# Kernel optimization log

Hardware: AMD Instinct MI355X
Metric: run time of the kernel (lower is better)

The kernel has to match this reference:

```python
import jax, jax.numpy as jnp
import numpy as np

B, S, D, H = 2, 2048, 1024, 16
HD = D // H


def setup_inputs() -> dict:
    key = jax.random.key(0)
    ks = jax.random.split(key, 7)
    scale = 1.0 / np.sqrt(D)
    x = jax.random.normal(ks[0], (B, S, D), dtype=jnp.float32)
    att_mask = jax.random.randint(ks[1], (B, S, S), 0, 2, dtype=jnp.int32)
    Wq = jax.random.normal(ks[2], (D, D), dtype=jnp.float32) * scale
    Wk = jax.random.normal(ks[3], (D, D), dtype=jnp.float32) * scale
    Wv = jax.random.normal(ks[4], (D, D), dtype=jnp.float32) * scale
    Wo = jax.random.normal(ks[5], (D, D), dtype=jnp.float32) * scale
    bo = jnp.zeros((D,), dtype=jnp.float32)
    return {"x": x, "att_mask": att_mask, "Wq": Wq, "Wk": Wk, "Wv": Wv, "Wo": Wo, "bo": bo}


def reference(x, att_mask, Wq, Wk, Wv, Wo, bo):
    # Self-attention: kv_source = x, kv_len = q_len = S
    b, s, d = x.shape
    # projections; weights stored as (d_in, d_out)
    q = (x @ Wq).reshape(b, s, H, HD).transpose(0, 2, 1, 3)  # (B,H,S,HD)
    k = (x @ Wk).reshape(b, s, H, HD).transpose(0, 2, 1, 3)
    v = (x @ Wv).reshape(b, s, H, HD).transpose(0, 2, 1, 3)

    scores = jnp.einsum("bhqd,bhkd->bhqk", q, k) / jnp.sqrt(jnp.float32(HD))
    mask = att_mask.astype(bool)[:, None, :, :]  # (B,1,S,S)
    scores = jnp.where(mask, scores, -jnp.inf)

    # Recover fully-masked rows: set their first column score to 0.0
    all_masked = jnp.all(jnp.isneginf(scores), axis=-1, keepdims=True)  # (B,H,S,1)
    first_col = jnp.arange(s) == 0  # (S,)
    scores = jnp.where(all_masked & first_col, 0.0, scores)

    weights = jax.nn.softmax(scores, axis=-1)  # dropout is identity in eval mode
    ctx = jnp.einsum("bhqk,bhkd->bhqd", weights, v)  # (B,H,S,HD)
    ctx = ctx.transpose(0, 2, 1, 3).reshape(b, s, d)
    return ctx @ Wo + bo
```

## Files before the change

kernel.cpp:

```cpp
#include <hip/hip_runtime.h>
#include <stdint.h>

typedef unsigned short u16;
typedef unsigned int u32;
typedef __attribute__((ext_vector_type(8))) short bf16x8;
typedef __attribute__((ext_vector_type(4))) float f32x4;
typedef __attribute__((ext_vector_type(4))) u32 u32x4;

#define MFMA16(a, b, c) __builtin_amdgcn_mfma_f32_16x16x32_bf16((a), (b), (c), 0, 0, 0)

#define QSCALE 0.18033688011112042f

__device__ __forceinline__ u16 f2bf(float f) {
  u32 u = __float_as_uint(f);
  u += 0x7fffu + ((u >> 16) & 1u);
  return (u16)(u >> 16);
}

__device__ __forceinline__ u32 cvt_pk_bf16(float a, float b) {
  u32 r;
  asm("v_cvt_pk_bf16_f32 %0, %1, %2" : "=v"(r) : "v"(a), "v"(b));
  return r;
}

__device__ __forceinline__ void load_lds16(const void* g, void* l) {
  __builtin_amdgcn_global_load_lds((const __attribute__((address_space(1))) void*)g,
                                   (__attribute__((address_space(3))) void*)l, 16, 0, 0);
}

__device__ __forceinline__ int swz8(int row, int cb) {
  return row * 128 + ((cb ^ (row & 7)) << 4);
}

__global__ __launch_bounds__(256) void prep_kernel(const float4* __restrict__ x,
                                                   const int* __restrict__ mask,
                                                   const float* __restrict__ W0,
                                                   const float* __restrict__ W1,
                                                   const float* __restrict__ W2,
                                                   const float* __restrict__ W3,
                                                   ushort4* __restrict__ xbf,
                                                   u16* __restrict__ wt,
                                                   u32* __restrict__ MB) {
  const int bid = blockIdx.x, tid = threadIdx.x;
  __shared__ float t[32][33];
  __shared__ u32 nib[4][64];
  if (bid < 1024) {
    for (int i = bid * 256 + tid; i < 1048576; i += 262144) {
      float4 v = x[i];
      ushort4 o;
      o.x = f2bf(v.x); o.y = f2bf(v.y); o.z = f2bf(v.z); o.w = f2bf(v.w);
      xbf[i] = o;
    }
  } else if (bid < 5120) {
    int r = bid - 1024;
    const int z = r >> 10; r &= 1023;
    const int by = (r >> 5) << 5, bx = (r & 31) << 5;
    const float* W = (z == 0) ? W0 : (z == 1) ? W1 : (z == 2) ? W2 : W3;
    u16* o = wt + (size_t)z * 1048576;
    const int tx = tid & 31, ty = tid >> 5;
#pragma unroll
    for (int j = 0; j < 32; j += 8) t[ty + j][tx] = W[(size_t)(by + ty + j) * 1024 + bx + tx];
    __syncthreads();
#pragma unroll
    for (int j = 0; j < 32; j += 8) o[(size_t)(bx + ty + j) * 1024 + by + tx] = f2bf(t[tx][ty + j]);
  } else {
    const int wave = tid >> 6, lane = tid & 63;
    const int gw = (bid - 5120) * 4 + wave;
    for (int r = gw; r < 32768; r += 4096) {
      const int row = r >> 3, kb = (r & 7) << 8;
      int4 v = *(const int4*)(mask + (size_t)row * 2048 + kb + lane * 4);
      nib[wave][lane] = (v.x ? 1u : 0u) | (v.y ? 2u : 0u) | (v.z ? 4u : 0u) | (v.w ? 8u : 0u);
      if (lane < 8) {
        const u32* p = &nib[wave][lane << 3];
        u32 a = p[0] | (p[1] << 4) | (p[2] << 8) | (p[3] << 12) |
                (p[4] << 16) | (p[5] << 20) | (p[6] << 24) | (p[7] << 28);
        MB[(size_t)row * 64 + (kb >> 5) + lane] = a;
      }
    }
  }
}

template <int MODE>
__global__ __launch_bounds__(256) void gemm_kernel(const u16* __restrict__ A,
                                                   const u16* __restrict__ Bt,
                                                   u16* __restrict__ Qo, u16* __restrict__ Ko,
                                                   u16* __restrict__ Vo, float* __restrict__ Fo,
                                                   const float* __restrict__ bias) {
  __shared__ u16 As[128 * 64];
  __shared__ u16 Bs[128 * 64];
  const int tid = threadIdx.x, lane = tid & 63;
  const int l15 = lane & 15, g = lane >> 4;
  const int wave = tid >> 6, wr = wave >> 1, wc = wave & 1;
  const int L = blockIdx.x;
  const int xcd = L & 7, bi = L >> 3;
  int m0, n0;
  if (MODE == 0) {
    m0 = (((xcd & 3) << 3) + (bi & 7)) * 128;
    n0 = ((xcd >> 2) * 12 + (bi >> 3)) * 128;
  } else {
    m0 = ((xcd << 2) + (bi & 3)) * 128;
    n0 = (bi >> 2) * 128;
  }
  const int xo = (((tid & 7) ^ ((tid >> 3) & 7)) << 4);
  const char* Ag = (const char*)A + (size_t)(m0 + (tid >> 3)) * 2048 + xo;
  const char* Bg = (const char*)Bt + (size_t)(n0 + (tid >> 3)) * 2048 + xo;
  char* Asc = (char*)As;
  char* Bsc = (char*)Bs;
  char* ldA = Asc + wave * 1024;
  char* ldB = Bsc + wave * 1024;

  f32x4 acc[4][4] = {};

  for (int kt = 0; kt < 16; ++kt) {
    const int kbyte = kt * 128;
    __syncthreads();
#pragma unroll
    for (int p = 0; p < 4; ++p) {
      load_lds16(Ag + kbyte + p * 65536, ldA + p * 4096);
      load_lds16(Bg + kbyte + p * 65536, ldB + p * 4096);
    }
    __syncthreads();

    bf16x8 af[4][2], bfr[4][2];
#pragma unroll
    for (int i = 0; i < 4; ++i) {
      const int ra = wr * 64 + i * 16 + l15;
      af[i][0] = *(const bf16x8*)(Asc + swz8(ra, g));
      af[i][1] = *(const bf16x8*)(Asc + swz8(ra, 4 + g));
    }
#pragma unroll
    for (int j = 0; j < 4; ++j) {
      const int rb = wc * 64 + j * 16 + l15;
      bfr[j][0] = *(const bf16x8*)(Bsc + swz8(rb, g));
      bfr[j][1] = *(const bf16x8*)(Bsc + swz8(rb, 4 + g));
    }
#pragma unroll
    for (int kk = 0; kk < 2; ++kk)
#pragma unroll
      for (int i = 0; i < 4; ++i)
#pragma unroll
        for (int j = 0; j < 4; ++j)
          acc[i][j] = MFMA16(af[i][kk], bfr[j][kk], acc[i][j]);
  }

  if (MODE == 1) {
#pragma unroll
    for (int i = 0; i < 4; ++i) {
      const int mrow = m0 + wr * 64 + i * 16 + g * 4;
#pragma unroll
      for (int j = 0; j < 4; ++j) {
        const int col = n0 + wc * 64 + j * 16 + l15;
        f32x4 v = acc[i][j];
#pragma unroll
        for (int r = 0; r < 4; ++r)
          Fo[(size_t)(mrow + r) * 1024 + col] = v[r] + bias[col];
      }
    }
  } else {
    const int which = n0 >> 10;
    const float scale = (which == 0) ? QSCALE : 1.0f;
    u16* outp = (which == 0) ? Qo : (which == 1) ? Ko : Vo;
#pragma unroll
    for (int i = 0; i < 4; ++i) {
      const int mrow = m0 + wr * 64 + i * 16 + g * 4;
      const int bb = mrow >> 11, s = mrow & 2047;
#pragma unroll
      for (int j = 0; j < 4; ++j) {
        const int col = (n0 + wc * 64 + j * 16 + l15) & 1023;
        const int h = col >> 6, hd = col & 63;
        f32x4 v = acc[i][j];
        if (which == 2) {
          const int qb = (s >> 2) & 15;
          const int half = (qb >> 2) & 1;
          const int chunk = (qb & 3) | ((qb & 8) >> 1);
          const int sp = (s & ~63) | (chunk << 3) | (half << 2);
          u32 w0 = cvt_pk_bf16(v[0], v[1]);
          u32 w1 = cvt_pk_bf16(v[2], v[3]);
          *(uint2*)(outp + ((((size_t)(bb * 16 + h)) * 64 + hd) * 2048 + sp)) = make_uint2(w0, w1);
        } else {
#pragma unroll
          for (int r = 0; r < 4; ++r)
            outp[(((size_t)(bb * 16 + h)) * 2048 + s + r) * 64 + hd] = f2bf(v[r] * scale);
        }
      }
    }
  }
}

__global__ __launch_bounds__(256, 2) void attn_kernel(const u16* __restrict__ Q,
                                                      const u16* __restrict__ K,
                                                      const u16* __restrict__ VT,
                                                      const u32* __restrict__ MB,
                                                      u16* __restrict__ CTX) {
  __shared__ u16 Kl[2][8192];
  __shared__ u16 Vl[2][8192];
  const int tid = threadIdx.x, lane = tid & 63, wave = tid >> 6;
  const int l15 = lane & 15, g = lane >> 4;
  const int L = blockIdx.x + (blockIdx.y << 4);
  const int bh = ((L & 7) << 2) + ((L >> 3) & 3);
  const int q0 = (L >> 5) * 128;
  const int b = bh >> 4, h = bh & 15;
  const int qw0 = q0 + wave * 32;

  const char* Qb = (const char*)Q + ((size_t)bh * 2048 + qw0) * 128;
  const bf16x8 aq00 = *(const bf16x8*)(Qb + l15 * 128 + g * 16);
  const bf16x8 aq01 = *(const bf16x8*)(Qb + l15 * 128 + 64 + g * 16);
  const bf16x8 aq10 = *(const bf16x8*)(Qb + (16 + l15) * 128 + g * 16);
  const bf16x8 aq11 = *(const bf16x8*)(Qb + (16 + l15) * 128 + 64 + g * 16);

  const char* Kg = (const char*)K + (size_t)bh * 2048 * 128;
  const char* Vg = (const char*)VT + (size_t)bh * 64 * 4096;
  const u32* mp0 = MB + ((size_t)b * 2048 + qw0 + l15) * 64;
  const u32* mp1 = mp0 + 16 * 64;

  const int lane8 = lane >> 3;
  const int xo = ((lane & 7) ^ lane8) << 4;
  const char* KsrcL = Kg + (size_t)lane8 * 128 + xo;
  const char* VsrcL = Vg + (size_t)lane8 * 4096 + xo;
  const int vhd = (wave & 1) * 32;
  const int vsub = wave >> 1;

  int koff[4][2], voff[2][4];
#pragma unroll
  for (int i = 0; i < 4; ++i) {
    koff[i][0] = swz8(i * 16 + l15, g);
    koff[i][1] = swz8(i * 16 + l15, 4 + g);
  }
#pragma unroll
  for (int ks = 0; ks < 2; ++ks)
#pragma unroll
    for (int j = 0; j < 4; ++j) voff[ks][j] = swz8(j * 16 + l15, ks * 4 + g);

  f32x4 oacc[4][2] = {};
  float lrow[2] = {0.f, 0.f};

  {
    char* Kd = (char*)Kl[0] + wave * 4096;
    char* Vd = (char*)Vl[0] + wave * 4096;
#pragma unroll
    for (int p = 0; p < 4; ++p) {
      load_lds16(KsrcL + wave * 4096 + p * 1024, Kd + p * 1024);
      load_lds16(VsrcL + (size_t)(vhd + p * 8) * 4096 + vsub * 128, Vd + p * 1024);
    }
  }
  uint4 mcA = *(const uint4*)mp0;
  uint4 mcB = *(const uint4*)mp1;
  __syncthreads();

  int cur = 0;
  for (int kb = 0; kb < 16; ++kb) {
    const int kn = (kb < 15) ? kb + 1 : 15;
    if (kb < 15) {
      char* Kd = (cur ? (char*)Kl[0] : (char*)Kl[1]) + wave * 4096;
      char* Vd = (cur ? (char*)Vl[0] : (char*)Vl[1]) + wave * 4096;
#pragma unroll
      for (int p = 0; p < 4; ++p) {
        load_lds16(KsrcL + (size_t)kn * 16384 + wave * 4096 + p * 1024, Kd + p * 1024);
        load_lds16(VsrcL + (size_t)(vhd + p * 8) * 4096 + (size_t)(2 * kn + vsub) * 128,
                   Vd + p * 1024);
      }
    }
    uint4 mnA = *(const uint4*)(mp0 + (size_t)kn * 4);
    uint4 mnB = *(const uint4*)(mp1 + (size_t)kn * 4);

#pragma unroll
    for (int s = 0; s < 2; ++s) {
      const char* Kc = (const char*)Kl[cur] + s * 8192;
      const char* Vc = (const char*)Vl[cur] + s * 8192;
      const u32 mA0 = s ? mcA.z : mcA.x, mA1 = s ? mcA.w : mcA.y;
      const u32 mB0 = s ? mcB.z : mcB.x, mB1 = s ? mcB.w : mcB.y;

      f32x4 sa[2][4];
      __builtin_amdgcn_s_setprio(1);
#pragma unroll
      for (int i = 0; i < 4; ++i) {
        const u32 wiA = ((i & 2) ? mA1 : mA0) >> ((i & 1) * 16 + g * 4);
        const u32 wiB = ((i & 2) ? mB1 : mB0) >> ((i & 1) * 16 + g * 4);
        f32x4 bA, bB;
#pragma unroll
        for (int r = 0; r < 4; ++r) {
          bA[r] = (wiA & (1u << r)) ? 0.f : -3e38f;
          bB[r] = (wiB & (1u << r)) ? 0.f : -3e38f;
        }
        bf16x8 bk0 = *(const bf16x8*)(Kc + koff[i][0]);
        bf16x8 bk1 = *(const bf16x8*)(Kc + koff[i][1]);
        sa[0][i] = MFMA16(bk1, aq01, MFMA16(bk0, aq00, bA));
        sa[1][i] = MFMA16(bk1, aq11, MFMA16(bk0, aq10, bB));
      }
      __builtin_amdgcn_s_setprio(0);

      u32 Wp[2][8];
#pragma unroll
      for (int f = 0; f < 2; ++f) {
        float ps = 0.f;
#pragma unroll
        for (int i = 0; i < 4; ++i) {
          const float p0 = __builtin_amdgcn_exp2f(sa[f][i][0]);
          const float p1 = __builtin_amdgcn_exp2f(sa[f][i][1]);
          const float p2 = __builtin_amdgcn_exp2f(sa[f][i][2]);
          const float p3 = __builtin_amdgcn_exp2f(sa[f][i][3]);
          ps += (p0 + p1) + (p2 + p3);
          Wp[f][i * 2] = cvt_pk_bf16(p0, p1);
          Wp[f][i * 2 + 1] = cvt_pk_bf16(p2, p3);
        }
        lrow[f] += ps;
      }

      __builtin_amdgcn_s_setprio(1);
#pragma unroll
      for (int ks = 0; ks < 2; ++ks) {
        u32x4 t0 = {Wp[0][ks * 4], Wp[0][ks * 4 + 1], Wp[0][ks * 4 + 2], Wp[0][ks * 4 + 3]};
        u32x4 t1 = {Wp[1][ks * 4], Wp[1][ks * 4 + 1], Wp[1][ks * 4 + 2], Wp[1][ks * 4 + 3]};
        const bf16x8 ap0 = __builtin_bit_cast(bf16x8, t0);
        const bf16x8 ap1 = __builtin_bit_cast(bf16x8, t1);
#pragma unroll
        for (int j = 0; j < 4; ++j) {
          bf16x8 bv = *(const bf16x8*)(Vc + voff[ks][j]);
          oacc[j][0] = MFMA16(bv, ap0, oacc[j][0]);
          oacc[j][1] = MFMA16(bv, ap1, oacc[j][1]);
        }
      }
      __builtin_amdgcn_s_setprio(0);
      __builtin_amdgcn_sched_barrier(0);
    }

    __syncthreads();
    cur ^= 1;
    mcA = mnA;
    mcB = mnB;
  }

#pragma unroll
  for (int f = 0; f < 2; ++f) {
    float lr = lrow[f];
    lr += __shfl_xor(lr, 16);
    lr += __shfl_xor(lr, 32);
    const float inv = 1.0f / fmaxf(lr, 1e-30f);
    u16* Cb = CTX + ((size_t)(b * 2048 + qw0 + f * 16 + l15)) * 1024 + h * 64 + g * 4;
#pragma unroll
    for (int j = 0; j < 4; ++j) {
      u32 w0 = cvt_pk_bf16(oacc[j][f][0] * inv, oacc[j][f][1] * inv);
      u32 w1 = cvt_pk_bf16(oacc[j][f][2] * inv, oacc[j][f][3] * inv);
      *(uint2*)(Cb + j * 16) = make_uint2(w0, w1);
    }
  }
}

extern "C" void kernel_launch(void* const* d_in, const int* in_sizes, int n_in,
                              void* d_out, int out_size, void* d_ws, size_t ws_size,
                              hipStream_t stream) {
  const float* x   = (const float*)d_in[0];
  const int* amask = (const int*)d_in[1];
  const float* Wq  = (const float*)d_in[2];
  const float* Wk  = (const float*)d_in[3];
  const float* Wv  = (const float*)d_in[4];
  const float* Wo  = (const float*)d_in[5];
  const float* bo  = (const float*)d_in[6];

  char* ws = (char*)d_ws;
  u16* xbf  = (u16*)(ws);
  u16* wt   = (u16*)(ws + 8388608);
  u16* Qb   = (u16*)(ws + 16777216);
  u16* Kb   = (u16*)(ws + 25165824);
  u16* VT   = (u16*)(ws + 33554432);
  u16* CTX  = (u16*)(ws + 41943040);
  u32* MB   = (u32*)(ws + 50331648);

  prep_kernel<<<6144, 256, 0, stream>>>((const float4*)x, amask, Wq, Wk, Wv, Wo,
                                        (ushort4*)xbf, wt, MB);

  gemm_kernel<0><<<768, 256, 0, stream>>>(xbf, wt, Qb, Kb, VT, nullptr, nullptr);

  attn_kernel<<<dim3(16, 32), 256, 0, stream>>>(Qb, Kb, VT, MB, CTX);

  gemm_kernel<1><<<256, 256, 0, stream>>>(CTX, wt + 3145728, nullptr, nullptr, nullptr,
                                          (float*)d_out, bo);
}
```

Measured before the change: 131.0 us.

## Move mask bit-packing into QKV GEMM launch, branchless mask bias, nontemporal mask loads

Mask packing moves out of the prep kernel into extra blocks of the QKV GEMM launch, so the bandwidth-bound mask read can overlap with the compute-bound GEMM blocks. The mask blocks reuse the GEMM's LDS as scratch and read the mask with nontemporal loads to avoid polluting the cache. In attention, the per-element mask bias select becomes a branchless bit-smear-and-mask that produces 0 or a large negative float. The gains depend on how the GEMM and mask blocks end up co-scheduled, and the mask blocks could delay GEMM tail blocks.

After: 133.1 us. No clear change (+1.6%).

```diff
diff --git a/kernel.cpp b/kernel.cpp
--- a/kernel.cpp
+++ b/kernel.cpp
@@ -6,10 +6,13 @@
 typedef __attribute__((ext_vector_type(8))) short bf16x8;
 typedef __attribute__((ext_vector_type(4))) float f32x4;
 typedef __attribute__((ext_vector_type(4))) u32 u32x4;
+typedef __attribute__((ext_vector_type(4))) int i32x4;
 
 #define MFMA16(a, b, c) __builtin_amdgcn_mfma_f32_16x16x32_bf16((a), (b), (c), 0, 0, 0)
 
 #define QSCALE 0.18033688011112042f
+
+#define BIT_SMEAR(x, r) ((u32)(((int)((x) << (31 - (r)))) >> 31))
 
 __device__ __forceinline__ u16 f2bf(float f) {
   u32 u = __float_as_uint(f);
@@ -33,17 +36,14 @@
 }
 
 __global__ __launch_bounds__(256) void prep_kernel(const float4* __restrict__ x,
-                                                   const int* __restrict__ mask,
                                                    const float* __restrict__ W0,
                                                    const float* __restrict__ W1,
                                                    const float* __restrict__ W2,
                                                    const float* __restrict__ W3,
                                                    ushort4* __restrict__ xbf,
-                                                   u16* __restrict__ wt,
-                                                   u32* __restrict__ MB) {
+                                                   u16* __restrict__ wt) {
   const int bid = blockIdx.x, tid = threadIdx.x;
   __shared__ float t[32][33];
-  __shared__ u32 nib[4][64];
   if (bid < 1024) {
     for (int i = bid * 256 + tid; i < 1048576; i += 262144) {
       float4 v = x[i];
@@ -51,7 +51,7 @@
       o.x = f2bf(v.x); o.y = f2bf(v.y); o.z = f2bf(v.z); o.w = f2bf(v.w);
       xbf[i] = o;
     }
-  } else if (bid < 5120) {
+  } else {
     int r = bid - 1024;
     const int z = r >> 10; r &= 1023;
     const int by = (r >> 5) << 5, bx = (r & 31) << 5;
@@ -63,29 +63,120 @@
     __syncthreads();
 #pragma unroll
     for (int j = 0; j < 32; j += 8) o[(size_t)(bx + ty + j) * 1024 + by + tx] = f2bf(t[tx][ty + j]);
-  } else {
+  }
+}
+
+__global__ __launch_bounds__(256) void gemm_qkv_kernel(const u16* __restrict__ A,
+                                                       const u16* __restrict__ Bt,
+                                                       const int* __restrict__ mask,
+                                                       u16* __restrict__ Qo,
+                                                       u16* __restrict__ Ko,
+                                                       u16* __restrict__ Vo,
+                                                       u32* __restrict__ MB) {
+  __shared__ u16 As[128 * 64];
+  __shared__ u16 Bs[128 * 64];
+  const int tid = threadIdx.x, bid = blockIdx.x;
+
+  if (bid >= 768) {
+    u32* nib = (u32*)As;
     const int wave = tid >> 6, lane = tid & 63;
-    const int gw = (bid - 5120) * 4 + wave;
+    const int gw = (bid - 768) * 4 + wave;
     for (int r = gw; r < 32768; r += 4096) {
       const int row = r >> 3, kb = (r & 7) << 8;
-      int4 v = *(const int4*)(mask + (size_t)row * 2048 + kb + lane * 4);
-      nib[wave][lane] = (v.x ? 1u : 0u) | (v.y ? 2u : 0u) | (v.z ? 4u : 0u) | (v.w ? 8u : 0u);
+      i32x4 v = __builtin_nontemporal_load((const i32x4*)(mask + (size_t)row * 2048 + kb) + lane);
+      nib[(wave << 6) + lane] =
+          (v.x ? 1u : 0u) | (v.y ? 2u : 0u) | (v.z ? 4u : 0u) | (v.w ? 8u : 0u);
       if (lane < 8) {
-        const u32* p = &nib[wave][lane << 3];
+        const u32* p = &nib[(wave << 6) + (lane << 3)];
         u32 a = p[0] | (p[1] << 4) | (p[2] << 8) | (p[3] << 12) |
                 (p[4] << 16) | (p[5] << 20) | (p[6] << 24) | (p[7] << 28);
         MB[(size_t)row * 64 + (kb >> 5) + lane] = a;
       }
     }
-  }
-}
-
-template <int MODE>
-__global__ __launch_bounds__(256) void gemm_kernel(const u16* __restrict__ A,
-                                                   const u16* __restrict__ Bt,
-                                                   u16* __restrict__ Qo, u16* __restrict__ Ko,
-                                                   u16* __restrict__ Vo, float* __restrict__ Fo,
-                                                   const float* __restrict__ bias) {
+    return;
+  }
+
+  const int lane = tid & 63;
+  const int l15 = lane & 15, g = lane >> 4;
+  const int wave = tid >> 6, wr = wave >> 1, wc = wave & 1;
+  const int xcd = bid & 7, bi = bid >> 3;
+  const int m0 = (((xcd & 3) << 3) + (bi & 7)) * 128;
+  const int n0 = ((xcd >> 2) * 12 + (bi >> 3)) * 128;
+  const int xo = (((tid & 7) ^ ((tid >> 3) & 7)) << 4);
+  const char* Ag = (const char*)A + (size_t)(m0 + (tid >> 3)) * 2048 + xo;
+  const char* Bg = (const char*)Bt + (size_t)(n0 + (tid >> 3)) * 2048 + xo;
+  char* Asc = (char*)As;
+  char* Bsc = (char*)Bs;
+  char* ldA = Asc + wave * 1024;
+  char* ldB = Bsc + wave * 1024;
+
+  f32x4 acc[4][4] = {};
+
+  for (int kt = 0; kt < 16; ++kt) {
+    const int kbyte = kt * 128;
+    __syncthreads();
+#pragma unroll
+    for (int p = 0; p < 4; ++p) {
+      load_lds16(Ag + kbyte + p * 65536, ldA + p * 4096);
+      load_lds16(Bg + kbyte + p * 65536, ldB + p * 4096);
+    }
+    __syncthreads();
+
+    bf16x8 af[4][2], bfr[4][2];
+#pragma unroll
+    for (int i = 0; i < 4; ++i) {
+      const int ra = wr * 64 + i * 16 + l15;
+      af[i][0] = *(const bf16x8*)(Asc + swz8(ra, g));
+      af[i][1] = *(const bf16x8*)(Asc + swz8(ra, 4 + g));
+    }
+#pragma unroll
+    for (int j = 0; j < 4; ++j) {
+      const int rb = wc * 64 + j * 16 + l15;
+      bfr[j][0] = *(const bf16x8*)(Bsc + swz8(rb, g));
+      bfr[j][1] = *(const bf16x8*)(Bsc + swz8(rb, 4 + g));
+    }
+#pragma unroll
+    for (int kk = 0; kk < 2; ++kk)
+#pragma unroll
+      for (int i = 0; i < 4; ++i)
+#pragma unroll
+        for (int j = 0; j < 4; ++j)
+          acc[i][j] = MFMA16(af[i][kk], bfr[j][kk], acc[i][j]);
+  }
+
+  const int which = n0 >> 10;
+  const float scale = (which == 0) ? QSCALE : 1.0f;
+  u16* outp = (which == 0) ? Qo : (which == 1) ? Ko : Vo;
+#pragma unroll
+  for (int i = 0; i < 4; ++i) {
+    const int mrow = m0 + wr * 64 + i * 16 + g * 4;
+    const int bb = mrow >> 11, s = mrow & 2047;
+#pragma unroll
+    for (int j = 0; j < 4; ++j) {
+      const int col = (n0 + wc * 64 + j * 16 + l15) & 1023;
+      const int h = col >> 6, hd = col & 63;
+      f32x4 v = acc[i][j];
+      if (which == 2) {
+        const int qb = (s >> 2) & 15;
+        const int half = (qb >> 2) & 1;
+        const int chunk = (qb & 3) | ((qb & 8) >> 1);
+        const int sp = (s & ~63) | (chunk << 3) | (half << 2);
+        u32 w0 = cvt_pk_bf16(v[0], v[1]);
+        u32 w1 = cvt_pk_bf16(v[2], v[3]);
+        *(uint2*)(outp + ((((size_t)(bb * 16 + h)) * 64 + hd) * 2048 + sp)) = make_uint2(w0, w1);
+      } else {
+#pragma unroll
+        for (int r = 0; r < 4; ++r)
+          outp[(((size_t)(bb * 16 + h)) * 2048 + s + r) * 64 + hd] = f2bf(v[r] * scale);
+      }
+    }
+  }
+}
+
+__global__ __launch_bounds__(256) void gemm_out_kernel(const u16* __restrict__ A,
+                                                       const u16* __restrict__ Bt,
+                                                       float* __restrict__ Fo,
+                                                       const float* __restrict__ bias) {
   __shared__ u16 As[128 * 64];
   __shared__ u16 Bs[128 * 64];
   const int tid = threadIdx.x, lane = tid & 63;
@@ -93,14 +184,8 @@
   const int wave = tid >> 6, wr = wave >> 1, wc = wave & 1;
   const int L = blockIdx.x;
   const int xcd = L & 7, bi = L >> 3;
-  int m0, n0;
-  if (MODE == 0) {
-    m0 = (((xcd & 3) << 3) + (bi & 7)) * 128;
-    n0 = ((xcd >> 2) * 12 + (bi >> 3)) * 128;
-  } else {
-    m0 = ((xcd << 2) + (bi & 3)) * 128;
-    n0 = (bi >> 2) * 128;
-  }
+  const int m0 = ((xcd << 2) + (bi & 3)) * 128;
+  const int n0 = (bi >> 2) * 128;
   const int xo = (((tid & 7) ^ ((tid >> 3) & 7)) << 4);
   const char* Ag = (const char*)A + (size_t)(m0 + (tid >> 3)) * 2048 + xo;
   const char* Bg = (const char*)Bt + (size_t)(n0 + (tid >> 3)) * 2048 + xo;
@@ -143,46 +228,16 @@
           acc[i][j] = MFMA16(af[i][kk], bfr[j][kk], acc[i][j]);
   }
 
-  if (MODE == 1) {
-#pragma unroll
-    for (int i = 0; i < 4; ++i) {
-      const int mrow = m0 + wr * 64 + i * 16 + g * 4;
-#pragma unroll
-      for (int j = 0; j < 4; ++j) {
-        const int col = n0 + wc * 64 + j * 16 + l15;
-        f32x4 v = acc[i][j];
-#pragma unroll
-        for (int r = 0; r < 4; ++r)
-          Fo[(size_t)(mrow + r) * 1024 + col] = v[r] + bias[col];
-      }
-    }
-  } else {
-    const int which = n0 >> 10;
-    const float scale = (which == 0) ? QSCALE : 1.0f;
-    u16* outp = (which == 0) ? Qo : (which == 1) ? Ko : Vo;
-#pragma unroll
-    for (int i = 0; i < 4; ++i) {
-      const int mrow = m0 + wr * 64 + i * 16 + g * 4;
-      const int bb = mrow >> 11, s = mrow & 2047;
-#pragma unroll
-      for (int j = 0; j < 4; ++j) {
-        const int col = (n0 + wc * 64 + j * 16 + l15) & 1023;
-        const int h = col >> 6, hd = col & 63;
-        f32x4 v = acc[i][j];
-        if (which == 2) {
-          const int qb = (s >> 2) & 15;
-          const int half = (qb >> 2) & 1;
-          const int chunk = (qb & 3) | ((qb & 8) >> 1);
-          const int sp = (s & ~63) | (chunk << 3) | (half << 2);
-          u32 w0 = cvt_pk_bf16(v[0], v[1]);
-          u32 w1 = cvt_pk_bf16(v[2], v[3]);
-          *(uint2*)(outp + ((((size_t)(bb * 16 + h)) * 64 + hd) * 2048 + sp)) = make_uint2(w0, w1);
-        } else {
-#pragma unroll
-          for (int r = 0; r < 4; ++r)
-            outp[(((size_t)(bb * 16 + h)) * 2048 + s + r) * 64 + hd] = f2bf(v[r] * scale);
-        }
-      }
+#pragma unroll
+  for (int i = 0; i < 4; ++i) {
+    const int mrow = m0 + wr * 64 + i * 16 + g * 4;
+#pragma unroll
+    for (int j = 0; j < 4; ++j) {
+      const int col = n0 + wc * 64 + j * 16 + l15;
+      f32x4 v = acc[i][j];
+#pragma unroll
+      for (int r = 0; r < 4; ++r)
+        Fo[(size_t)(mrow + r) * 1024 + col] = v[r] + bias[col];
     }
   }
 }
@@ -274,13 +329,14 @@
       __builtin_amdgcn_s_setprio(1);
 #pragma unroll
       for (int i = 0; i < 4; ++i) {
-        const u32 wiA = ((i & 2) ? mA1 : mA0) >> ((i & 1) * 16 + g * 4);
-        const u32 wiB = ((i & 2) ? mB1 : mB0) >> ((i & 1) * 16 + g * 4);
+        const int sh = (i & 1) * 16 + g * 4;
+        const u32 invA = ~(((i & 2) ? mA1 : mA0) >> sh);
+        const u32 invB = ~(((i & 2) ? mB1 : mB0) >> sh);
         f32x4 bA, bB;
 #pragma unroll
         for (int r = 0; r < 4; ++r) {
-          bA[r] = (wiA & (1u << r)) ? 0.f : -3e38f;
-          bB[r] = (wiB & (1u << r)) ? 0.f : -3e38f;
+          bA[r] = __int_as_float(BIT_SMEAR(invA, r) & 0xFF7F0000u);
+          bB[r] = __int_as_float(BIT_SMEAR(invB, r) & 0xFF7F0000u);
         }
         bf16x8 bk0 = *(const bf16x8*)(Kc + koff[i][0]);
         bf16x8 bk1 = *(const bf16x8*)(Kc + koff[i][1]);
@@ -366,13 +422,12 @@
   u16* CTX  = (u16*)(ws + 41943040);
   u32* MB   = (u32*)(ws + 50331648);
 
-  prep_kernel<<<6144, 256, 0, stream>>>((const float4*)x, amask, Wq, Wk, Wv, Wo,
-                                        (ushort4*)xbf, wt, MB);
-
-  gemm_kernel<0><<<768, 256, 0, stream>>>(xbf, wt, Qb, Kb, VT, nullptr, nullptr);
+  prep_kernel<<<5120, 256, 0, stream>>>((const float4*)x, Wq, Wk, Wv, Wo,
+                                        (ushort4*)xbf, wt);
+
+  gemm_qkv_kernel<<<1792, 256, 0, stream>>>(xbf, wt, amask, Qb, Kb, VT, MB);
 
   attn_kernel<<<dim3(16, 32), 256, 0, stream>>>(Qb, Kb, VT, MB, CTX);
 
-  gemm_kernel<1><<<256, 256, 0, stream>>>(CTX, wt + 3145728, nullptr, nullptr, nullptr,
-                                          (float*)d_out, bo);
-}
+  gemm_out_kernel<<<256, 256, 0, stream>>>(CTX, wt + 3145728, (float*)d_out, bo);
+}
```
